# Performance work log

Hardware: AMD Instinct MI355X
Metric: run time of the kernel (lower is better)

The kernel has to match this reference:

```python
import jax, jax.numpy as jnp
import numpy as np

B, S, E, H = 4, 2048, 1024, 16
D = E // H  # d_k = 64
NEG = -1000000000.0  # matches torch masked_fill constant


def setup_inputs() -> dict:
    rk = jax.random.key(0)
    kq, kk, kv, km = jax.random.split(rk, 4)
    query = jax.random.normal(kq, (B, S, E), dtype=jnp.float32)
    key = jax.random.normal(kk, (B, S, E), dtype=jnp.float32)
    value = jax.random.normal(kv, (B, S, E), dtype=jnp.float32)
    mask = jax.random.randint(km, (B, S, S), 0, 2, dtype=jnp.int32)
    return {"query": query, "key": key, "value": value, "mask": mask}


def _split_heads(x):
    # (B, S, E) -> (B, H, S, D)
    return x.reshape(B, S, H, D).transpose(0, 2, 1, 3)


def reference(query, key, value, mask):
    q = _split_heads(query)
    k = _split_heads(key)
    v = _split_heads(value)
    scale = np.float32(1.0 / np.sqrt(D))
    scores = jnp.einsum('bhqd,bhkd->bhqk', q, k) * scale  # (B,H,S,S)
    scores = jnp.where(mask[:, None, :, :] == 0, jnp.float32(NEG), scores)
    weights = jax.nn.softmax(scores, axis=-1)
    attn = jnp.einsum('bhqk,bhkd->bhqd', weights, v)  # (B,H,S,D)
    concat = attn.transpose(0, 2, 1, 3).reshape(B, S, E)
    return concat
```

## Files before the change

kernel.cpp:

```cpp
#include <hip/hip_runtime.h>
#include <hip/hip_bf16.h>
#include <math.h>

constexpr int B = 4, S = 2048, E = 1024, H = 16, D = 64;
constexpr float NEGF = -1000000000.0f;
constexpr float KSCALE = 0.125f * 1.44269504f;

typedef __attribute__((ext_vector_type(8))) short short8;
typedef __attribute__((ext_vector_type(16))) float f32x16;

__device__ inline short f2bf(float x) {
    __hip_bfloat16 h = __float2bfloat16(x);
    return *reinterpret_cast<short*>(&h);
}
__device__ inline unsigned pk(float a, float b) {
    return (unsigned)(unsigned short)f2bf(a) | ((unsigned)(unsigned short)f2bf(b) << 16);
}
__device__ inline void gl_lds16(const void* g, void* l) {
    __builtin_amdgcn_global_load_lds(
        (const __attribute__((address_space(1))) unsigned int*)g,
        (__attribute__((address_space(3))) unsigned int*)l, 16, 0, 0);
}

constexpr size_t WS_K  = 0;
constexpr size_t WS_VT = 18874368;
constexpr size_t WS_MB = 37748736;
constexpr size_t WS_NEED = 39845888;

__global__ void prep_all(const float* __restrict__ K, const float* __restrict__ V,
                         const int* __restrict__ M, char* __restrict__ ws) {
    __shared__ float Vf[64][69];
    const int bid = blockIdx.x, tid = threadIdx.x;

    {
        int g = bid * 256 + tid;
        int rowd = g >> 2, qtr = g & 3;
        int b = rowd >> 15, h = (rowd >> 11) & 15, s = rowd & 2047;
        const float* p = K + ((size_t)(b * S + s)) * E + h * 64 + qtr * 16;
        float4 v0 = *(const float4*)(p + 0),  v1 = *(const float4*)(p + 4);
        float4 v2 = *(const float4*)(p + 8),  v3 = *(const float4*)(p + 12);
        uint4 o0, o1;
        o0.x = pk(v0.x * KSCALE, v0.y * KSCALE); o0.y = pk(v0.z * KSCALE, v0.w * KSCALE);
        o0.z = pk(v1.x * KSCALE, v1.y * KSCALE); o0.w = pk(v1.z * KSCALE, v1.w * KSCALE);
        o1.x = pk(v2.x * KSCALE, v2.y * KSCALE); o1.y = pk(v2.z * KSCALE, v2.w * KSCALE);
        o1.z = pk(v3.x * KSCALE, v3.y * KSCALE); o1.w = pk(v3.z * KSCALE, v3.w * KSCALE);
        char* d = ws + WS_K + (size_t)rowd * 144 + qtr * 32;
        *(uint4*)d = o0; *(uint4*)(d + 16) = o1;
    }

    {
        int bh = bid >> 5, kt = bid & 31;
        int b = bh >> 4, h = bh & 15;
        {
            int r = tid >> 2, c4 = (tid & 3) * 16;
            const float* p = V + ((size_t)(b * S + kt * 64 + r)) * E + h * 64 + c4;
            float4 a = *(const float4*)(p + 0), bb = *(const float4*)(p + 4);
            float4 c = *(const float4*)(p + 8), dd = *(const float4*)(p + 12);
            *(float4*)&Vf[r][c4 + 0] = a;  *(float4*)&Vf[r][c4 + 4] = bb;
            *(float4*)&Vf[r][c4 + 8] = c;  *(float4*)&Vf[r][c4 + 12] = dd;
        }
        __syncthreads();
        int d = tid >> 2, sq = (tid & 3) * 16;
        float v[16];
#pragma unroll
        for (int i = 0; i < 16; ++i) v[i] = Vf[sq + i][d];
        uint4 o0, o1;
        o0.x = pk(v[0], v[1]);   o0.y = pk(v[2], v[3]);
        o0.z = pk(v[4], v[5]);   o0.w = pk(v[6], v[7]);
        o1.x = pk(v[8], v[9]);   o1.y = pk(v[10], v[11]);
        o1.z = pk(v[12], v[13]); o1.w = pk(v[14], v[15]);
        char* o = ws + WS_VT + ((size_t)(bh * 32 + kt)) * 9216 + d * 144 + sq * 2;
        *(uint4*)o = o0; *(uint4*)(o + 16) = o1;
    }

    {
        unsigned long long* Mb = (unsigned long long*)(ws + WS_MB);
        const int lane = tid & 63;
        const int wid = bid * 4 + (tid >> 6);
#pragma unroll
        for (int it = 0; it < 8; ++it) {
            const size_t base = ((size_t)wid * 8 + it) * 256;
            int4 mv = *(const int4*)(M + base + lane * 4);
            unsigned nib = (mv.x != 0 ? 1u : 0u) | (mv.y != 0 ? 2u : 0u)
                         | (mv.z != 0 ? 4u : 0u) | (mv.w != 0 ? 8u : 0u);
            unsigned s1 = nib | ((unsigned)__shfl_xor((int)nib, 1, 64) << 4);
            unsigned s2 = s1 | ((unsigned)__shfl_xor((int)s1, 2, 64) << 8);
            unsigned s3 = s2 | ((unsigned)__shfl_xor((int)s2, 4, 64) << 16);
            unsigned hi = (unsigned)__shfl_xor((int)s3, 8, 64);
            if ((lane & 15) == 0) {
                unsigned long long wv = (unsigned long long)s3 | ((unsigned long long)hi << 32);
                Mb[base / 64 + (lane >> 4)] = wv;
            }
        }
    }
}

__global__ __launch_bounds__(256, 4)
void fa_mfma(const float* __restrict__ Q, const char* __restrict__ ws,
             const unsigned long long* __restrict__ Mb, float* __restrict__ O) {
    __shared__ char smem[36864];
    const int tid = threadIdx.x;
    const int w = tid >> 6, lane = tid & 63;
    const int L5 = lane & 31, h6 = lane >> 5;
    const int sh4 = h6 * 4;
    const int h = blockIdx.x & 15, b = (blockIdx.x >> 4) & 3, qt = blockIdx.x >> 6;
    const int bh = b * 16 + h;
    const int q0w = qt * 128 + w * 32;

    const char* Kws  = ws + WS_K;
    const char* Vtws = ws + WS_VT;

    short8 qf[4];
#pragma unroll
    for (int ks = 0; ks < 4; ++ks) {
        const float* qp = Q + ((size_t)(b * S + q0w + L5)) * E
                            + h * 64 + ks * 16 + h6 * 8;
        float4 a = *(const float4*)qp;
        float4 c = *(const float4*)(qp + 4);
        uint4 u;
        u.x = pk(a.x, a.y); u.y = pk(a.z, a.w);
        u.z = pk(c.x, c.y); u.w = pk(c.z, c.w);
        qf[ks] = *(short8*)&u;
    }

    f32x16 acc[2];
#pragma unroll
    for (int mb = 0; mb < 2; ++mb) acc[mb] = (f32x16)0.0f;
    float l0 = 0.0f;
    const int qA = q0w + L5;

    {
        const char* ksrc = Kws + ((size_t)bh * S) * 144;
        const char* vsrc = Vtws + ((size_t)bh * 32) * 9216;
#pragma unroll
        for (int c = 0; c < 5; ++c) {
            int idx = c * 4 + w;
            if (idx < 18) {
                int off = idx * 1024;
                const char* g = (off < 9216) ? (ksrc + off) : (vsrc + off - 9216);
                gl_lds16(g + lane * 16, smem + off);
            }
        }
    }

    for (int ti = 0; ti < 32; ++ti) {
        __syncthreads();

        if (ti + 1 < 32) {
            const char* ksrc = Kws + ((size_t)bh * S + (ti + 1) * 64) * 144;
            const char* vsrc = Vtws + ((size_t)(bh * 32 + ti + 1)) * 9216;
            char* dst = smem + ((ti + 1) & 1) * 18432;
#pragma unroll
            for (int c = 0; c < 5; ++c) {
                int idx = c * 4 + w;
                if (idx < 18) {
                    int off = idx * 1024;
                    const char* g = (off < 9216) ? (ksrc + off) : (vsrc + off - 9216);
                    gl_lds16(g + lane * 16, dst + off);
                }
            }
        }
        const unsigned long long mA = Mb[((size_t)b * S + qA) * 32 + ti];

        const char* Ks = smem + (ti & 1) * 18432;
        const char* Vt = Ks + 9216;

#pragma unroll
        for (int mbK = 0; mbK < 2; ++mbK) {
            short8 kf[4];
#pragma unroll
            for (int ks = 0; ks < 4; ++ks)
                kf[ks] = *(const short8*)(Ks + (mbK * 32 + L5) * 144 + ks * 32 + h6 * 16);
            const unsigned wm = (unsigned)(mA >> (mbK * 32)) >> sh4;

            f32x16 s = (f32x16)0.0f;
#pragma unroll
            for (int ks = 0; ks < 4; ++ks)
                s = __builtin_amdgcn_mfma_f32_32x32x16_bf16(kf[ks], qf[ks], s, 0, 0, 0);

            float lacc = 0.0f;
            unsigned pd[8];
#pragma unroll
            for (int i = 0; i < 8; ++i) {
                const int r0i = 2 * i, r1i = 2 * i + 1;
                const int kc0 = (r0i & 3) + 8 * (r0i >> 2);
                const int kc1 = (r1i & 3) + 8 * (r1i >> 2);
                float e0 = __builtin_amdgcn_exp2f(s[r0i]);
                float e1 = __builtin_amdgcn_exp2f(s[r1i]);
                e0 = ((wm >> kc0) & 1u) ? e0 : 0.0f;
                e1 = ((wm >> kc1) & 1u) ? e1 : 0.0f;
                lacc += e0 + e1;
                pd[i] = pk(e0, e1);
            }
            l0 += lacc;

            short8 pf[2];
#pragma unroll
            for (int sub = 0; sub < 2; ++sub) {
                const unsigned dA = pd[4 * sub + 0], dB = pd[4 * sub + 1];
                const unsigned dC = pd[4 * sub + 2], dD = pd[4 * sub + 3];
                const unsigned t0 = h6 ? dA : dC;
                const unsigned t1 = h6 ? dB : dD;
                const unsigned r0 = (unsigned)__shfl_xor((int)t0, 32, 64);
                const unsigned r1 = (unsigned)__shfl_xor((int)t1, 32, 64);
                uint4 u;
                u.x = h6 ? r0 : dA;  u.y = h6 ? r1 : dB;
                u.z = h6 ? dC : r0;  u.w = h6 ? dD : r1;
                pf[sub] = *(short8*)&u;
            }

#pragma unroll
            for (int mbV = 0; mbV < 2; ++mbV) {
#pragma unroll
                for (int sub = 0; sub < 2; ++sub) {
                    short8 vf = *(const short8*)(Vt + (mbV * 32 + L5) * 144
                                                 + (mbK * 2 + sub) * 32 + h6 * 16);
                    acc[mbV] = __builtin_amdgcn_mfma_f32_32x32x16_bf16(
                        vf, pf[sub], acc[mbV], 0, 0, 0);
                }
            }
        }
    }

    l0 += __shfl_xor(l0, 32, 64);
    const float inv = 1.0f / l0;
    __syncthreads();
    float* ep = (float*)(smem + w * 4608);
#pragma unroll
    for (int mb = 0; mb < 2; ++mb) {
#pragma unroll
        for (int r = 0; r < 16; ++r) {
            const int d = (r & 3) + 8 * (r >> 2) + sh4;
            ep[L5 * 36 + d] = acc[mb][r] * inv;
        }
        __builtin_amdgcn_s_waitcnt(0xc07f);
        const int row = lane >> 1, c = (lane & 1) * 16;
#pragma unroll
        for (int i = 0; i < 4; ++i) {
            float4 t = *(const float4*)&ep[row * 36 + c + 4 * i];
            *(float4*)(O + ((size_t)(b * S + q0w + row)) * E
                         + h * 64 + mb * 32 + c + 4 * i) = t;
        }
        __builtin_amdgcn_s_waitcnt(0xc07f);
    }
}

constexpr int QT = 64, KT = 64, LD = D + 4;
constexpr float SCALE = 0.125f;
__global__ __launch_bounds__(256, 3)
void fa_fp32(const float* __restrict__ Q, const float* __restrict__ K,
             const float* __restrict__ V, const int* __restrict__ M,
             float* __restrict__ Out)
{
    __shared__ float Qs[QT][LD];
    __shared__ float Vs[KT][LD];
    __shared__ float KPs[KT][LD];
    const int tid = threadIdx.x, tx = tid & 15, ty = tid >> 4;
    const int bid = blockIdx.x;
    const int h = bid % H, b = (bid / H) % B, qt = bid / (H * B);
    const int q0 = qt * QT;
    {
        const int col = tx * 4;
#pragma unroll
        for (int i = 0; i < 4; ++i) {
            const int row = ty + i * 16;
            *(float4*)&Qs[row][col] = *(const float4*)&Q[((size_t)(b * S + q0 + row)) * E + h * D + col];
        }
    }
    const int qr0 = ty * 4, d0 = tx * 4;
    float acc[4][4] = {};
    float m_i[4], l_i[4];
#pragma unroll
    for (int j = 0; j < 4; ++j) { m_i[j] = -INFINITY; l_i[j] = 0.0f; }
    for (int kt = 0; kt < S; kt += KT) {
        __syncthreads();
        {
            const int col = tx * 4;
#pragma unroll
            for (int i = 0; i < 4; ++i) {
                const int row = ty + i * 16;
                const size_t g = ((size_t)(b * S + kt + row)) * E + h * D + col;
                *(float4*)&KPs[row][col] = *(const float4*)&K[g];
                *(float4*)&Vs[row][col] = *(const float4*)&V[g];
            }
        }
        __syncthreads();
        float s[4][4] = {};
#pragma unroll
        for (int d = 0; d < D; d += 4) {
            float4 a[4], bb[4];
#pragma unroll
            for (int j = 0; j < 4; ++j) a[j] = *(const float4*)&Qs[qr0 + j][d];
#pragma unroll
            for (int i = 0; i < 4; ++i) bb[i] = *(const float4*)&KPs[tx + 16 * i][d];
#pragma unroll
            for (int j = 0; j < 4; ++j)
#pragma unroll
                for (int i = 0; i < 4; ++i)
                    s[j][i] += a[j].x * bb[i].x + a[j].y * bb[i].y + a[j].z * bb[i].z + a[j].w * bb[i].w;
        }
#pragma unroll
        for (int j = 0; j < 4; ++j) {
            const int* mrow = &M[((size_t)b * S + (q0 + qr0 + j)) * S + kt];
#pragma unroll
            for (int i = 0; i < 4; ++i) {
                const int mk = mrow[tx + 16 * i];
                s[j][i] = mk ? s[j][i] * SCALE : NEGF;
            }
        }
#pragma unroll
        for (int j = 0; j < 4; ++j) {
            float tm = fmaxf(fmaxf(s[j][0], s[j][1]), fmaxf(s[j][2], s[j][3]));
#pragma unroll
            for (int off = 8; off; off >>= 1) tm = fmaxf(tm, __shfl_xor(tm, off, 16));
            const float nm = fmaxf(m_i[j], tm);
            const float alpha = __expf(m_i[j] - nm);
            m_i[j] = nm;
            float rs = 0.0f;
#pragma unroll
            for (int i = 0; i < 4; ++i) { const float p = __expf(s[j][i] - nm); s[j][i] = p; rs += p; }
#pragma unroll
            for (int off = 8; off; off >>= 1) rs += __shfl_xor(rs, off, 16);
            l_i[j] = l_i[j] * alpha + rs;
#pragma unroll
            for (int dd = 0; dd < 4; ++dd) acc[j][dd] *= alpha;
        }
        __syncthreads();
#pragma unroll
        for (int j = 0; j < 4; ++j)
#pragma unroll
            for (int i = 0; i < 4; ++i) KPs[qr0 + j][tx + 16 * i] = s[j][i];
        __syncthreads();
#pragma unroll 4
        for (int kk = 0; kk < KT; kk += 4) {
            float4 p[4], vv[4];
#pragma unroll
            for (int j = 0; j < 4; ++j) p[j] = *(const float4*)&KPs[qr0 + j][kk];
#pragma unroll
            for (int u = 0; u < 4; ++u) vv[u] = *(const float4*)&Vs[kk + u][d0];
#pragma unroll
            for (int j = 0; j < 4; ++j) {
                acc[j][0] += p[j].x * vv[0].x + p[j].y * vv[1].x + p[j].z * vv[2].x + p[j].w * vv[3].x;
                acc[j][1] += p[j].x * vv[0].y + p[j].y * vv[1].y + p[j].z * vv[2].y + p[j].w * vv[3].y;
                acc[j][2] += p[j].x * vv[0].z + p[j].y * vv[1].z + p[j].z * vv[2].z + p[j].w * vv[3].z;
                acc[j][3] += p[j].x * vv[0].w + p[j].y * vv[1].w + p[j].z * vv[2].w + p[j].w * vv[3].w;
            }
        }
    }
#pragma unroll
    for (int j = 0; j < 4; ++j) {
        const float iv = 1.0f / l_i[j];
        float4 r;
        r.x = acc[j][0] * iv; r.y = acc[j][1] * iv; r.z = acc[j][2] * iv; r.w = acc[j][3] * iv;
        *(float4*)&Out[((size_t)(b * S + q0 + qr0 + j)) * E + h * D + d0] = r;
    }
}

extern "C" void kernel_launch(void* const* d_in, const int* in_sizes, int n_in,
                              void* d_out, int out_size, void* d_ws, size_t ws_size,
                              hipStream_t stream) {
    (void)in_sizes; (void)n_in; (void)out_size;
    const float* q = (const float*)d_in[0];
    const float* k = (const float*)d_in[1];
    const float* v = (const float*)d_in[2];
    const int*   m = (const int*)d_in[3];
    float* out = (float*)d_out;

    if (ws_size >= WS_NEED) {
        char* ws = (char*)d_ws;
        prep_all<<<2048, 256, 0, stream>>>(k, v, m, ws);
        fa_mfma<<<1024, 256, 0, stream>>>(q, ws,
            (const unsigned long long*)(ws + WS_MB), out);
    } else {
        fa_fp32<<<B * H * (S / QT), 256, 0, stream>>>(q, k, v, m, out);
    }
}
```

Measured before the change: 305.0 us.

## Store mask as byte masks and apply via perm-AND on packed bf16 probabilities

The mask is now pre-expanded to one byte per element, interleaved so each lane loads its 32 mask bytes with two 16-byte loads per tile. In the softmax loop the bf16-packed exponentials are ANDed with perm-built 16-bit masks, and the row sum is taken from the packed bf16 values, which removes the per-element bit tests and selects. The float-to-bf16 conversion is replaced with a round-half-up add plus byte perm, which is cheaper than the library helper but is not round-to-nearest-even. In exchange the mask workspace grows eightfold (from 2 MB to 16 MB), so the prep kernel writes and the attention kernel reads much more mask data; the prep kernel also zero-fills the padding at the end of each K and V row.

```diff
diff --git a/kernel.cpp b/kernel.cpp
--- a/kernel.cpp
+++ b/kernel.cpp
@@ -9,12 +9,10 @@
 typedef __attribute__((ext_vector_type(8))) short short8;
 typedef __attribute__((ext_vector_type(16))) float f32x16;
 
-__device__ inline short f2bf(float x) {
-    __hip_bfloat16 h = __float2bfloat16(x);
-    return *reinterpret_cast<short*>(&h);
-}
-__device__ inline unsigned pk(float a, float b) {
-    return (unsigned)(unsigned short)f2bf(a) | ((unsigned)(unsigned short)f2bf(b) << 16);
+__device__ inline unsigned pk2(float a, float b) {
+    unsigned ua = __builtin_bit_cast(unsigned, a) + 0x8000u;
+    unsigned ub = __builtin_bit_cast(unsigned, b) + 0x8000u;
+    return __builtin_amdgcn_perm(ub, ua, 0x07060302u);
 }
 __device__ inline void gl_lds16(const void* g, void* l) {
     __builtin_amdgcn_global_load_lds(
@@ -25,7 +23,7 @@
 constexpr size_t WS_K  = 0;
 constexpr size_t WS_VT = 18874368;
 constexpr size_t WS_MB = 37748736;
-constexpr size_t WS_NEED = 39845888;
+constexpr size_t WS_NEED = 54525952;
 
 __global__ void prep_all(const float* __restrict__ K, const float* __restrict__ V,
                          const int* __restrict__ M, char* __restrict__ ws) {
@@ -40,12 +38,16 @@
         float4 v0 = *(const float4*)(p + 0),  v1 = *(const float4*)(p + 4);
         float4 v2 = *(const float4*)(p + 8),  v3 = *(const float4*)(p + 12);
         uint4 o0, o1;
-        o0.x = pk(v0.x * KSCALE, v0.y * KSCALE); o0.y = pk(v0.z * KSCALE, v0.w * KSCALE);
-        o0.z = pk(v1.x * KSCALE, v1.y * KSCALE); o0.w = pk(v1.z * KSCALE, v1.w * KSCALE);
-        o1.x = pk(v2.x * KSCALE, v2.y * KSCALE); o1.y = pk(v2.z * KSCALE, v2.w * KSCALE);
-        o1.z = pk(v3.x * KSCALE, v3.y * KSCALE); o1.w = pk(v3.z * KSCALE, v3.w * KSCALE);
+        o0.x = pk2(v0.x * KSCALE, v0.y * KSCALE); o0.y = pk2(v0.z * KSCALE, v0.w * KSCALE);
+        o0.z = pk2(v1.x * KSCALE, v1.y * KSCALE); o0.w = pk2(v1.z * KSCALE, v1.w * KSCALE);
+        o1.x = pk2(v2.x * KSCALE, v2.y * KSCALE); o1.y = pk2(v2.z * KSCALE, v2.w * KSCALE);
+        o1.z = pk2(v3.x * KSCALE, v3.y * KSCALE); o1.w = pk2(v3.z * KSCALE, v3.w * KSCALE);
         char* d = ws + WS_K + (size_t)rowd * 144 + qtr * 32;
         *(uint4*)d = o0; *(uint4*)(d + 16) = o1;
+        if (qtr == 3) {
+            uint4 z; z.x = z.y = z.z = z.w = 0;
+            *(uint4*)(d + 32) = z;
+        }
     }
 
     {
@@ -65,61 +67,58 @@
 #pragma unroll
         for (int i = 0; i < 16; ++i) v[i] = Vf[sq + i][d];
         uint4 o0, o1;
-        o0.x = pk(v[0], v[1]);   o0.y = pk(v[2], v[3]);
-        o0.z = pk(v[4], v[5]);   o0.w = pk(v[6], v[7]);
-        o1.x = pk(v[8], v[9]);   o1.y = pk(v[10], v[11]);
-        o1.z = pk(v[12], v[13]); o1.w = pk(v[14], v[15]);
+        o0.x = pk2(v[0], v[1]);   o0.y = pk2(v[2], v[3]);
+        o0.z = pk2(v[4], v[5]);   o0.w = pk2(v[6], v[7]);
+        o1.x = pk2(v[8], v[9]);   o1.y = pk2(v[10], v[11]);
+        o1.z = pk2(v[12], v[13]); o1.w = pk2(v[14], v[15]);
         char* o = ws + WS_VT + ((size_t)(bh * 32 + kt)) * 9216 + d * 144 + sq * 2;
         *(uint4*)o = o0; *(uint4*)(o + 16) = o1;
-    }
-
-    {
-        unsigned long long* Mb = (unsigned long long*)(ws + WS_MB);
-        const int lane = tid & 63;
-        const int wid = bid * 4 + (tid >> 6);
+        if (sq == 48) {
+            uint4 z; z.x = z.y = z.z = z.w = 0;
+            *(uint4*)(o + 32) = z;
+        }
+    }
+
+    {
+        unsigned* Mb = (unsigned*)(ws + WS_MB);
+        const int t = bid * 256 + tid;
 #pragma unroll
         for (int it = 0; it < 8; ++it) {
-            const size_t base = ((size_t)wid * 8 + it) * 256;
-            int4 mv = *(const int4*)(M + base + lane * 4);
-            unsigned nib = (mv.x != 0 ? 1u : 0u) | (mv.y != 0 ? 2u : 0u)
-                         | (mv.z != 0 ? 4u : 0u) | (mv.w != 0 ? 8u : 0u);
-            unsigned s1 = nib | ((unsigned)__shfl_xor((int)nib, 1, 64) << 4);
-            unsigned s2 = s1 | ((unsigned)__shfl_xor((int)s1, 2, 64) << 8);
-            unsigned s3 = s2 | ((unsigned)__shfl_xor((int)s2, 4, 64) << 16);
-            unsigned hi = (unsigned)__shfl_xor((int)s3, 8, 64);
-            if ((lane & 15) == 0) {
-                unsigned long long wv = (unsigned long long)s3 | ((unsigned long long)hi << 32);
-                Mb[base / 64 + (lane >> 4)] = wv;
-            }
+            int gidx = it * 524288 + t;
+            int4 mv = *((const int4*)M + gidx);
+            unsigned d = (mv.x ? 0xFFu : 0u) | (mv.y ? 0xFF00u : 0u)
+                       | (mv.z ? 0xFF0000u : 0u) | (mv.w ? 0xFF000000u : 0u);
+            int row = gidx >> 4, g = gidx & 15;
+            Mb[row * 16 + (g & 1) * 8 + (g >> 1)] = d;
         }
     }
 }
 
 __global__ __launch_bounds__(256, 4)
 void fa_mfma(const float* __restrict__ Q, const char* __restrict__ ws,
-             const unsigned long long* __restrict__ Mb, float* __restrict__ O) {
+             float* __restrict__ O) {
     __shared__ char smem[36864];
     const int tid = threadIdx.x;
     const int w = tid >> 6, lane = tid & 63;
     const int L5 = lane & 31, h6 = lane >> 5;
-    const int sh4 = h6 * 4;
     const int h = blockIdx.x & 15, b = (blockIdx.x >> 4) & 3, qt = blockIdx.x >> 6;
     const int bh = b * 16 + h;
     const int q0w = qt * 128 + w * 32;
 
     const char* Kws  = ws + WS_K;
     const char* Vtws = ws + WS_VT;
+    const int qA = q0w + L5;
+    const char* mrow = ws + WS_MB + ((size_t)(b * S + qA)) * 2048 + h6 * 32;
 
     short8 qf[4];
 #pragma unroll
     for (int ks = 0; ks < 4; ++ks) {
-        const float* qp = Q + ((size_t)(b * S + q0w + L5)) * E
-                            + h * 64 + ks * 16 + h6 * 8;
+        const float* qp = Q + ((size_t)(b * S + qA)) * E + h * 64 + ks * 16 + h6 * 8;
         float4 a = *(const float4*)qp;
         float4 c = *(const float4*)(qp + 4);
         uint4 u;
-        u.x = pk(a.x, a.y); u.y = pk(a.z, a.w);
-        u.z = pk(c.x, c.y); u.w = pk(c.z, c.w);
+        u.x = pk2(a.x, a.y); u.y = pk2(a.z, a.w);
+        u.z = pk2(c.x, c.y); u.w = pk2(c.z, c.w);
         qf[ks] = *(short8*)&u;
     }
 
@@ -127,7 +126,6 @@
 #pragma unroll
     for (int mb = 0; mb < 2; ++mb) acc[mb] = (f32x16)0.0f;
     float l0 = 0.0f;
-    const int qA = q0w + L5;
 
     {
         const char* ksrc = Kws + ((size_t)bh * S) * 144;
@@ -160,7 +158,10 @@
                 }
             }
         }
-        const unsigned long long mA = Mb[((size_t)b * S + qA) * 32 + ti];
+        const uint4 mlo = *(const uint4*)(mrow + ti * 64);
+        const uint4 mhi = *(const uint4*)(mrow + ti * 64 + 16);
+        const unsigned mdw[8] = {mlo.x, mlo.y, mlo.z, mlo.w,
+                                 mhi.x, mhi.y, mhi.z, mhi.w};
 
         const char* Ks = smem + (ti & 1) * 18432;
         const char* Vt = Ks + 9216;
@@ -171,7 +172,6 @@
 #pragma unroll
             for (int ks = 0; ks < 4; ++ks)
                 kf[ks] = *(const short8*)(Ks + (mbK * 32 + L5) * 144 + ks * 32 + h6 * 16);
-            const unsigned wm = (unsigned)(mA >> (mbK * 32)) >> sh4;
 
             f32x16 s = (f32x16)0.0f;
 #pragma unroll
@@ -182,15 +182,17 @@
             unsigned pd[8];
 #pragma unroll
             for (int i = 0; i < 8; ++i) {
-                const int r0i = 2 * i, r1i = 2 * i + 1;
-                const int kc0 = (r0i & 3) + 8 * (r0i >> 2);
-                const int kc1 = (r1i & 3) + 8 * (r1i >> 2);
-                float e0 = __builtin_amdgcn_exp2f(s[r0i]);
-                float e1 = __builtin_amdgcn_exp2f(s[r1i]);
-                e0 = ((wm >> kc0) & 1u) ? e0 : 0.0f;
-                e1 = ((wm >> kc1) & 1u) ? e1 : 0.0f;
-                lacc += e0 + e1;
-                pd[i] = pk(e0, e1);
+                float e0 = __builtin_amdgcn_exp2f(s[2 * i]);
+                float e1 = __builtin_amdgcn_exp2f(s[2 * i + 1]);
+                unsigned pm = pk2(e0, e1);
+                const unsigned mv = mdw[mbK * 4 + (i >> 1)];
+                const unsigned am = __builtin_amdgcn_perm(
+                    mv, mv, (i & 1) ? 0x03030202u : 0x01010000u);
+                pm &= am;
+                pd[i] = pm;
+                float lo = __builtin_bit_cast(float, pm << 16);
+                float hi = __builtin_bit_cast(float, pm & 0xFFFF0000u);
+                lacc += lo + hi;
             }
             l0 += lacc;
 
@@ -230,7 +232,7 @@
     for (int mb = 0; mb < 2; ++mb) {
 #pragma unroll
         for (int r = 0; r < 16; ++r) {
-            const int d = (r & 3) + 8 * (r >> 2) + sh4;
+            const int d = (r & 3) + 8 * (r >> 2) + h6 * 4;
             ep[L5 * 36 + d] = acc[mb][r] * inv;
         }
         __builtin_amdgcn_s_waitcnt(0xc07f);
@@ -369,8 +371,7 @@
     if (ws_size >= WS_NEED) {
         char* ws = (char*)d_ws;
         prep_all<<<2048, 256, 0, stream>>>(k, v, m, ws);
-        fa_mfma<<<1024, 256, 0, stream>>>(q, ws,
-            (const unsigned long long*)(ws + WS_MB), out);
+        fa_mfma<<<1024, 256, 0, stream>>>(q, ws, out);
     } else {
         fa_fp32<<<B * H * (S / QT), 256, 0, stream>>>(q, k, v, m, out);
     }
```

Measured after the change: 300.8 us. About the same (-1.4%).
